# Optimization experiments

Measured on AMD Instinct MI355X. Metric: run time of the kernel, lower is better.

## Reference

```python
import jax, jax.numpy as jnp
import numpy as np
import math
from jax import lax

B, C, L = 8, 512, 1024
NCONV, K, H = 4, 7, 8
DH = C // H
EPS = 1e-5
NEG = -1e30


def layer_norm(x, g, b):
    mu = jnp.mean(x, axis=-1, keepdims=True)
    var = jnp.mean(jnp.square(x - mu), axis=-1, keepdims=True)
    return (x - mu) * lax.rsqrt(var + EPS) * g + b


def positional_encoding(d, n):
    pos = jnp.arange(n, dtype=jnp.float32)[:, None]                     # [n,1]
    div = jnp.exp(jnp.arange(0, d, 2, dtype=jnp.float32) * (-math.log(10000.0) / d))
    ang = pos * div                                                      # [n,d/2]
    pe = jnp.zeros((d, n), dtype=jnp.float32)
    pe = pe.at[0::2].set(jnp.sin(ang).T).at[1::2].set(jnp.cos(ang).T)
    return pe                                                            # [d,n]


def setup_inputs() -> dict:
    key = jax.random.key(0)
    ks = jax.random.split(key, 20)
    s = 0.02
    inp = {
        "x": jax.random.normal(ks[0], (B, C, L), jnp.float32),
        "mask": jnp.ones((B, L), jnp.float32),
        # conv stack params (stacked over NCONV layers)
        "dw_w": jax.random.normal(ks[1], (NCONV, C, 1, K), jnp.float32) * s,
        "dw_b": jnp.zeros((NCONV, C), jnp.float32),
        "pw_w": jax.random.normal(ks[2], (NCONV, C, C), jnp.float32) * s,
        "pw_b": jnp.zeros((NCONV, C), jnp.float32),
        "ln_conv_g": jnp.ones((NCONV, C), jnp.float32),
        "ln_conv_b": jnp.zeros((NCONV, C), jnp.float32),
        # attention params (torch Linear layout: [out,in])
        "Wq": jax.random.normal(ks[3], (C, C), jnp.float32) * s,
        "bq": jnp.zeros((C,), jnp.float32),
        "Wk": jax.random.normal(ks[4], (C, C), jnp.float32) * s,
        "bk": jnp.zeros((C,), jnp.float32),
        "Wv": jax.random.normal(ks[5], (C, C), jnp.float32) * s,
        "bv": jnp.zeros((C,), jnp.float32),
        "Wo": jax.random.normal(ks[6], (C, C), jnp.float32) * s,
        "bo": jnp.zeros((C,), jnp.float32),
        "ln_att_g": jnp.ones((C,), jnp.float32),
        "ln_att_b": jnp.zeros((C,), jnp.float32),
        # final fc + its layernorm
        "Wf": jax.random.normal(ks[7], (C, C), jnp.float32) * s,
        "bf": jnp.zeros((C,), jnp.float32),
        "ln_fc_g": jnp.ones((C,), jnp.float32),
        "ln_fc_b": jnp.zeros((C,), jnp.float32),
    }
    return inp


def reference(x, mask, dw_w, dw_b, pw_w, pw_b, ln_conv_g, ln_conv_b,
              Wq, bq, Wk, bk, Wv, bv, Wo, bo, ln_att_g, ln_att_b,
              Wf, bf, ln_fc_g, ln_fc_b):
    # positional encoding on channels-first input, then -> [B,L,C]
    out = x + positional_encoding(C, L)[None]          # [B,C,L]; dropout = eval mode (identity)
    out = out.transpose(0, 2, 1)                       # [B,L,C]
    res = out
    for i in range(NCONV):                             # fixed small layer loop
        h = layer_norm(out, ln_conv_g[i], ln_conv_b[i])
        h = h.transpose(0, 2, 1)                       # [B,C,L]
        h = lax.conv_general_dilated(h, dw_w[i], (1,), [(K // 2, K // 2)],
                                     dimension_numbers=("NCH", "OIH", "NCH"),
                                     feature_group_count=C) + dw_b[i][None, :, None]
        h = jnp.einsum("bcl,oc->bol", h, pw_w[i]) + pw_b[i][None, :, None]
        h = jax.nn.relu(h).transpose(0, 2, 1)          # [B,L,C]
        out = h + res
        res = out
    # masked multi-head self-attention
    a = layer_norm(out, ln_att_g, ln_att_b)
    q = (a @ Wq.T + bq).reshape(B, L, H, DH)
    k = (a @ Wk.T + bk).reshape(B, L, H, DH)
    v = (a @ Wv.T + bv).reshape(B, L, H, DH)
    scale = 1.0 / math.sqrt(DH)
    scores = jnp.einsum("blhd,bmhd->bhlm", q, k) * scale   # [B,H,L,L]
    m = mask[:, None, None, :]                              # mask over keys
    scores = scores * m + (1.0 - m) * NEG
    attn = jax.nn.softmax(scores, axis=-1)
    o = jnp.einsum("bhlm,bmhd->blhd", attn, v).reshape(B, L, C)
    o = o @ Wo.T + bo
    out = o + res
    res = out
    # feed-forward (single Linear + relu) with residual
    f = layer_norm(out, ln_fc_g, ln_fc_b)
    f = jax.nn.relu(f @ Wf.T + bf)
    out = f + res
    return out
```

## Files before the change

### kernel.cpp

```cpp
#include <hip/hip_runtime.h>
#include <hip/hip_bf16.h>

#define L_SEQ 1024
#define CCH   512
#define NB    8

typedef __bf16 bf16_t;
typedef __bf16 bf16x4 __attribute__((ext_vector_type(4)));
typedef __bf16 bf16x8 __attribute__((ext_vector_type(8)));
typedef float  f32x4  __attribute__((ext_vector_type(4)));

__device__ __forceinline__ void gload_lds16(const void* g, void* l) {
  __builtin_amdgcn_global_load_lds((const __attribute__((address_space(1))) void*)g,
                                   (__attribute__((address_space(3))) void*)l, 16, 0, 0);
}

__global__ __launch_bounds__(256) void cvtall_kernel(
    const float* __restrict__ pw_w, const float* __restrict__ Wq,
    const float* __restrict__ Wk, const float* __restrict__ Wv,
    const float* __restrict__ Wo, const float* __restrict__ Wf,
    const float* __restrict__ dw_w,
    bf16_t* __restrict__ WPW, bf16_t* __restrict__ WQKV,
    bf16_t* __restrict__ WOB, bf16_t* __restrict__ WFB,
    float* __restrict__ WT) {
  int idx = blockIdx.x * 256 + threadIdx.x;
  if (idx < 1048576) { WPW[idx] = (bf16_t)pw_w[idx]; return; }
  idx -= 1048576;
  if (idx < 262144) { WQKV[idx] = (bf16_t)Wq[idx]; return; }
  idx -= 262144;
  if (idx < 262144) { WQKV[262144 + idx] = (bf16_t)Wk[idx]; return; }
  idx -= 262144;
  if (idx < 262144) { WQKV[524288 + idx] = (bf16_t)Wv[idx]; return; }
  idx -= 262144;
  if (idx < 262144) { WOB[idx] = (bf16_t)Wo[idx]; return; }
  idx -= 262144;
  if (idx < 262144) { WFB[idx] = (bf16_t)Wf[idx]; return; }
  idx -= 262144;
  if (idx < 14336) {
    int i = idx / 3584, r = idx % 3584, t = r >> 9, c = r & 511;
    WT[idx] = dw_w[i * 3584 + c * 7 + t];
  }
}

__global__ __launch_bounds__(256) void pet_kernel(float* __restrict__ PET) {
  int idx = blockIdx.x * 256 + threadIdx.x;
  int l = idx >> 9, c = idx & 511;
  float div = expf(-(float)(2 * (c >> 1)) * (9.210340371976184f / 512.0f));
  float ang = (float)l * div;
  PET[idx] = (c & 1) ? cosf(ang) : sinf(ang);
}

__global__ __launch_bounds__(256) void pe_kernel(const float* __restrict__ x,
                                                 const float* __restrict__ PET,
                                                 float* __restrict__ out) {
  __shared__ float tile[32][33];
  int l0 = blockIdx.x * 32, c0 = blockIdx.y * 32, b = blockIdx.z;
  int tx = threadIdx.x, ty = threadIdx.y;
#pragma unroll
  for (int r = 0; r < 32; r += 8)
    tile[ty + r][tx] = x[(size_t)(b * CCH + c0 + ty + r) * L_SEQ + l0 + tx];
  __syncthreads();
#pragma unroll
  for (int r = 0; r < 32; r += 8) {
    int l = l0 + ty + r, c = c0 + tx;
    out[(size_t)(b * L_SEQ + l) * CCH + c] = tile[tx][ty + r] + PET[l * CCH + c];
  }
}

__global__ __launch_bounds__(256) void stats_kernel(const float* __restrict__ in,
                                                    float* __restrict__ Psum,
                                                    float* __restrict__ Psq) {
  int w = threadIdx.x >> 6, l = threadIdx.x & 63;
  int row = blockIdx.x * 4 + w;
  const float* p = in + (size_t)row * CCH + l * 8;
  float v[8];
  *(float4*)(&v[0]) = *(const float4*)p;
  *(float4*)(&v[4]) = *(const float4*)(p + 4);
  float s = 0.f, q = 0.f;
#pragma unroll
  for (int j = 0; j < 8; j++) { s += v[j]; q += v[j] * v[j]; }
  s += __shfl_xor(s, 1); q += __shfl_xor(q, 1);
  s += __shfl_xor(s, 2); q += __shfl_xor(q, 2);
  s += __shfl_xor(s, 4); q += __shfl_xor(q, 4);
  if ((l & 7) == 0) {
    Psum[row * 8 + (l >> 3)] = s;
    Psq[row * 8 + (l >> 3)] = q;
  }
}

__global__ __launch_bounds__(256) void ln_apply_kernel(const float* __restrict__ in,
                                                       const float* __restrict__ Psum,
                                                       const float* __restrict__ Psq,
                                                       const float* __restrict__ gam,
                                                       const float* __restrict__ bet,
                                                       bf16_t* __restrict__ out) {
  int w = threadIdx.x >> 6, l = threadIdx.x & 63;
  int row = blockIdx.x * 4 + w;
  float v0 = 0.f;
  if (l < 8) v0 = Psum[row * 8 + l];
  else if (l < 16) v0 = Psq[row * 8 + (l - 8)];
  v0 += __shfl_xor(v0, 1); v0 += __shfl_xor(v0, 2); v0 += __shfl_xor(v0, 4);
  float sum = __shfl(v0, 0), sq = __shfl(v0, 8);
  float mean = sum * (1.0f / 512.0f);
  float var = sq * (1.0f / 512.0f) - mean * mean;
  float inv = rsqrtf(var + 1e-5f);
  const float* p = in + (size_t)row * CCH + l * 8;
  float v[8], gv[8], bv[8];
  *(float4*)(&v[0]) = *(const float4*)p;
  *(float4*)(&v[4]) = *(const float4*)(p + 4);
  *(float4*)(&gv[0]) = *(const float4*)(gam + l * 8);
  *(float4*)(&gv[4]) = *(const float4*)(gam + l * 8 + 4);
  *(float4*)(&bv[0]) = *(const float4*)(bet + l * 8);
  *(float4*)(&bv[4]) = *(const float4*)(bet + l * 8 + 4);
  bf16x8 o;
#pragma unroll
  for (int j = 0; j < 8; j++) o[j] = (bf16_t)((v[j] - mean) * inv * gv[j] + bv[j]);
  *(bf16x8*)(out + (size_t)row * CCH + l * 8) = o;
}

__global__ __launch_bounds__(256) void dwln_kernel(const float* __restrict__ in,
                                                   const float* __restrict__ Psum,
                                                   const float* __restrict__ Psq,
                                                   const float* __restrict__ gam,
                                                   const float* __restrict__ bet,
                                                   const float* __restrict__ wtt,
                                                   const float* __restrict__ dbias,
                                                   bf16_t* __restrict__ out) {
  int idx = blockIdx.x * 256 + threadIdx.x;
  int lane = threadIdx.x & 63;
  int row = idx >> 6;
  int l = row & (L_SEQ - 1);
  float m_ = 0.f, i_ = 0.f;
  if (lane < 7) {
    int ll = l + lane - 3;
    if (ll >= 0 && ll < L_SEQ) {
      int rr = row + lane - 3;
      float s = 0.f, q = 0.f;
#pragma unroll
      for (int c = 0; c < 8; c++) { s += Psum[rr * 8 + c]; q += Psq[rr * 8 + c]; }
      float mm = s * (1.0f / 512.0f);
      m_ = mm;
      i_ = rsqrtf(q * (1.0f / 512.0f) - mm * mm + 1e-5f);
    }
  }
  float gv[8], bv[8], acc[8];
  *(float4*)&gv[0] = *(const float4*)(gam + lane * 8);
  *(float4*)&gv[4] = *(const float4*)(gam + lane * 8 + 4);
  *(float4*)&bv[0] = *(const float4*)(bet + lane * 8);
  *(float4*)&bv[4] = *(const float4*)(bet + lane * 8 + 4);
  *(float4*)&acc[0] = *(const float4*)(dbias + lane * 8);
  *(float4*)&acc[4] = *(const float4*)(dbias + lane * 8 + 4);
#pragma unroll
  for (int t = 0; t < 7; t++) {
    float mt = __shfl(m_, t), it = __shfl(i_, t);
    int ll = l + t - 3;
    if (ll >= 0 && ll < L_SEQ) {
      const float* p = in + (size_t)(row + t - 3) * CCH + lane * 8;
      float v[8], wv[8];
      *(float4*)&v[0] = *(const float4*)p;
      *(float4*)&v[4] = *(const float4*)(p + 4);
      *(float4*)&wv[0] = *(const float4*)(wtt + t * CCH + lane * 8);
      *(float4*)&wv[4] = *(const float4*)(wtt + t * CCH + lane * 8 + 4);
#pragma unroll
      for (int j = 0; j < 8; j++)
        acc[j] += ((v[j] - mt) * it * gv[j] + bv[j]) * wv[j];
    }
  }
  bf16x8 o;
#pragma unroll
  for (int j = 0; j < 8; j++) o[j] = (bf16_t)acc[j];
  *(bf16x8*)&out[(size_t)row * CCH + lane * 8] = o;
}

#define GEMM_STAGE(SRCA, SRCB, BI, K0)                                            \
  do {                                                                            \
    _Pragma("unroll") for (int cc = 0; cc < 2; cc++) {                            \
      int row_ = cc * 32 + w * 8 + srow;                                          \
      int off_ = (scb ^ ((row_ & 7) << 4)) >> 1;                                  \
      gload_lds16(SRCA + (size_t)(m0 + row_) * CCH + (K0) + off_,                 \
                  &As[BI][(cc * 32 + w * 8) * 64]);                               \
    }                                                                             \
    _Pragma("unroll") for (int cc = 0; cc < 4; cc++) {                            \
      int row_ = cc * 32 + w * 8 + srow;                                          \
      int off_ = (scb ^ ((row_ & 7) << 4)) >> 1;                                  \
      gload_lds16(SRCB + (size_t)(n0 + row_) * CCH + (K0) + off_,                 \
                  &Bs[BI][(cc * 32 + w * 8) * 64]);                               \
    }                                                                             \
  } while (0)

#define GEMM_COMPUTE(BI)                                                          \
  do {                                                                            \
    _Pragma("unroll") for (int ks = 0; ks < 2; ks++) {                            \
      bf16x8 fa[2], fb[4];                                                        \
      _Pragma("unroll") for (int i = 0; i < 2; i++) {                             \
        int ra = wr * 32 + i * 16 + lc;                                           \
        fa[i] = *(const bf16x8*)&As[BI][ra * 64 +                                 \
                 (((ks * 64 + lg * 16) ^ ((ra & 7) << 4)) >> 1)];                 \
      }                                                                           \
      _Pragma("unroll") for (int j = 0; j < 4; j++) {                             \
        int rb = wc * 64 + j * 16 + lc;                                           \
        fb[j] = *(const bf16x8*)&Bs[BI][rb * 64 +                                 \
                 (((ks * 64 + lg * 16) ^ ((rb & 7) << 4)) >> 1)];                 \
      }                                                                           \
      _Pragma("unroll") for (int i = 0; i < 2; i++)                               \
        _Pragma("unroll") for (int j = 0; j < 4; j++)                             \
          acc[i][j] = __builtin_amdgcn_mfma_f32_16x16x32_bf16(fa[i], fb[j],       \
                                                              acc[i][j], 0, 0, 0);\
    }                                                                             \
  } while (0)

template <int RELU, int RES, int BF16OUT, int STATS>
__global__ __launch_bounds__(256) void gemm_kernel(const bf16_t* __restrict__ A,
                                                   const bf16_t* __restrict__ W,
                                                   const float* __restrict__ bias,
                                                   const float* __restrict__ res,
                                                   float* __restrict__ outf,
                                                   bf16_t* __restrict__ outb,
                                                   float* __restrict__ Psum,
                                                   float* __restrict__ Psq) {
  __shared__ __align__(16) bf16_t As[2][64 * 64];
  __shared__ __align__(16) bf16_t Bs[2][128 * 64];
  int tid = threadIdx.x;
  int w = tid >> 6, l = tid & 63;
  int m0 = blockIdx.x * 64, n0 = blockIdx.y * 128;
  int wr = w >> 1, wc = w & 1;
  int lc = l & 15, lg = l >> 4;
  int srow = l >> 3, scb = (l & 7) * 16;
  f32x4 acc[2][4];
#pragma unroll
  for (int i = 0; i < 2; i++)
#pragma unroll
    for (int j = 0; j < 4; j++) acc[i][j] = f32x4{0.f, 0.f, 0.f, 0.f};

  GEMM_STAGE(A, W, 0, 0);
  __syncthreads();
  int cur = 0;
  for (int t = 0; t < 8; t++) {
    if (t < 7) GEMM_STAGE(A, W, cur ^ 1, (t + 1) * 64);
    GEMM_COMPUTE(cur);
    __syncthreads();
    cur ^= 1;
  }

  float ps[2][4], pq[2][4];
  if (STATS) {
#pragma unroll
    for (int i = 0; i < 2; i++)
#pragma unroll
      for (int r = 0; r < 4; r++) { ps[i][r] = 0.f; pq[i][r] = 0.f; }
  }
#pragma unroll
  for (int i = 0; i < 2; i++) {
    int mbase = m0 + wr * 32 + i * 16 + lg * 4;
#pragma unroll
    for (int j = 0; j < 4; j++) {
      int n = n0 + wc * 64 + j * 16 + lc;
      float bn = bias[n];
#pragma unroll
      for (int r = 0; r < 4; r++) {
        int m = mbase + r;
        float v2 = acc[i][j][r] + bn;
        if (RELU) v2 = fmaxf(v2, 0.f);
        if (RES) v2 += res[(size_t)m * CCH + n];
        if (BF16OUT) outb[(size_t)m * CCH + n] = (bf16_t)v2;
        else outf[(size_t)m * CCH + n] = v2;
        if (STATS) { ps[i][r] += v2; pq[i][r] += v2 * v2; }
      }
    }
  }
  if (STATS) {
    int chunk = blockIdx.y * 2 + wc;
#pragma unroll
    for (int i = 0; i < 2; i++)
#pragma unroll
      for (int r = 0; r < 4; r++) {
        float s = ps[i][r], q = pq[i][r];
        s += __shfl_xor(s, 1); q += __shfl_xor(q, 1);
        s += __shfl_xor(s, 2); q += __shfl_xor(q, 2);
        s += __shfl_xor(s, 4); q += __shfl_xor(q, 4);
        s += __shfl_xor(s, 8); q += __shfl_xor(q, 8);
        if (lc == 0) {
          int row = m0 + wr * 32 + i * 16 + lg * 4 + r;
          Psum[row * 8 + chunk] = s;
          Psq[row * 8 + chunk] = q;
        }
      }
  }
}

__global__ __launch_bounds__(256) void qkv_kernel(const bf16_t* __restrict__ A,
                                                  const bf16_t* __restrict__ Wqkv,
                                                  const float* __restrict__ bq,
                                                  const float* __restrict__ bk,
                                                  const float* __restrict__ bv,
                                                  bf16_t* __restrict__ QB,
                                                  bf16_t* __restrict__ KB,
                                                  bf16_t* __restrict__ VT) {
  __shared__ __align__(16) bf16_t As[2][64 * 64];
  __shared__ __align__(16) bf16_t Bs[2][128 * 64];
  int tid = threadIdx.x;
  int w = tid >> 6, l = tid & 63;
  int m0 = blockIdx.x * 64, n0 = blockIdx.y * 128;
  int sec = n0 >> 9;
  int wr = w >> 1, wc = w & 1;
  int lc = l & 15, lg = l >> 4;
  int srow = l >> 3, scb = (l & 7) * 16;
  f32x4 acc[2][4];
#pragma unroll
  for (int i = 0; i < 2; i++)
#pragma unroll
    for (int j = 0; j < 4; j++) acc[i][j] = f32x4{0.f, 0.f, 0.f, 0.f};

  GEMM_STAGE(A, Wqkv, 0, 0);
  __syncthreads();
  int cur = 0;
  for (int t = 0; t < 8; t++) {
    if (t < 7) GEMM_STAGE(A, Wqkv, cur ^ 1, (t + 1) * 64);
    GEMM_COMPUTE(cur);
    __syncthreads();
    cur ^= 1;
  }

  const float* bp = (sec == 0) ? bq : (sec == 1) ? bk : bv;
#pragma unroll
  for (int i = 0; i < 2; i++) {
    int mbase = m0 + wr * 32 + i * 16 + lg * 4;
#pragma unroll
    for (int j = 0; j < 4; j++) {
      int n = n0 + wc * 64 + j * 16 + lc;
      int nl = n & 511;
      float bn = bp[nl];
      if (sec < 2) {
        bf16_t* ob = (sec == 0) ? QB : KB;
#pragma unroll
        for (int r = 0; r < 4; r++)
          ob[(size_t)(mbase + r) * CCH + nl] = (bf16_t)(acc[i][j][r] + bn);
      } else {
        int h = nl >> 6, d = nl & 63;
        int b = mbase >> 10, lpos = mbase & 1023;
        bf16x4 t;
#pragma unroll
        for (int r = 0; r < 4; r++) t[r] = (bf16_t)(acc[i][j][r] + bn);
        *(bf16x4*)&VT[(((size_t)(b * 8 + h) * 64 + d) * L_SEQ) + lpos] = t;
      }
    }
  }
}

__global__ __launch_bounds__(256) void attn_kernel(const bf16_t* __restrict__ Q,
                                                   const bf16_t* __restrict__ K,
                                                   const bf16_t* __restrict__ VT,
                                                   const float* __restrict__ mask,
                                                   bf16_t* __restrict__ O) {
  __shared__ __align__(16) bf16_t Ks[64 * 64];
  __shared__ __align__(16) bf16_t Vs[64 * 64];
  __shared__ __align__(16) bf16_t Pl[4][16 * 64];
  int tid = threadIdx.x;
  int w = tid >> 6, l = tid & 63;
  int bid = blockIdx.x;
  int sw = (bid & 7) * 64 + (bid >> 3);
  int qb = sw & 7, h = (sw >> 3) & 7, b = sw >> 6;
  int lg = l >> 4, lc = l & 15;

  bf16x8 qf[2][2];
#pragma unroll
  for (int s = 0; s < 2; s++) {
    int qrow = qb * 128 + s * 64 + w * 16 + lc;
    const bf16_t* qptr = Q + ((size_t)(b * L_SEQ + qrow) * CCH + h * 64);
    qf[s][0] = *(const bf16x8*)(qptr + lg * 8);
    qf[s][1] = *(const bf16x8*)(qptr + 32 + lg * 8);
  }

  f32x4 oacc[2][4];
  float psl[2][4];
#pragma unroll
  for (int s = 0; s < 2; s++)
#pragma unroll
    for (int nf = 0; nf < 4; nf++) {
      oacc[s][nf] = f32x4{0.f, 0.f, 0.f, 0.f};
      psl[s][nf] = 0.f;
    }

  int srow = l >> 3;
  int scb = (l & 7) * 16;

  for (int kc = 0; kc < 16; kc++) {
#pragma unroll
    for (int r = 0; r < 2; r++) {
      int row = r * 32 + w * 8 + srow;
      int sc = (scb ^ ((row & 7) << 4)) >> 1;
      int key = kc * 64 + row;
      gload_lds16(K + ((size_t)(b * L_SEQ + key) * CCH + h * 64 + sc),
                  &Ks[(r * 32 + w * 8) * 64]);
      gload_lds16(VT + (((size_t)(b * 8 + h) * 64 + row) * L_SEQ + kc * 64 + sc),
                  &Vs[(r * 32 + w * 8) * 64]);
    }
    __syncthreads();

    float mv[4];
#pragma unroll
    for (int kf = 0; kf < 4; kf++) mv[kf] = mask[b * L_SEQ + kc * 64 + kf * 16 + lc];

#pragma unroll
    for (int s = 0; s < 2; s++) {
      f32x4 sacc[4];
#pragma unroll
      for (int kf = 0; kf < 4; kf++) sacc[kf] = f32x4{0.f, 0.f, 0.f, 0.f};
      __builtin_amdgcn_s_setprio(1);
#pragma unroll
      for (int kf = 0; kf < 4; kf++) {
        int row = kf * 16 + lc;
        int sx = (row & 7) << 4;
        const bf16_t* kr = &Ks[row * 64];
        bf16x8 b0 = *(const bf16x8*)(kr + (((lg * 16) ^ sx) >> 1));
        sacc[kf] = __builtin_amdgcn_mfma_f32_16x16x32_bf16(qf[s][0], b0, sacc[kf], 0, 0, 0);
        bf16x8 b1 = *(const bf16x8*)(kr + (((64 + lg * 16) ^ sx) >> 1));
        sacc[kf] = __builtin_amdgcn_mfma_f32_16x16x32_bf16(qf[s][1], b1, sacc[kf], 0, 0, 0);
      }
      __builtin_amdgcn_s_setprio(0);

#pragma unroll
      for (int kf = 0; kf < 4; kf++) {
        float mneg = (1.f - mv[kf]) * (-1e30f);
        float msc = 0.125f * mv[kf];
#pragma unroll
        for (int j = 0; j < 4; j++) {
          float p = __expf(sacc[kf][j] * msc + mneg);
          psl[s][j] += p;
          int q = lg * 4 + j;
          int cb = (kf * 32 + lc * 2) ^ ((q & 7) << 4);
          Pl[w][(q * 128 + cb) >> 1] = (bf16_t)p;
        }
      }

      int sp = (lc & 7) << 4;
      bf16x8 pa0 = *(const bf16x8*)&Pl[w][(lc * 128 + ((lg * 16) ^ sp)) >> 1];
      bf16x8 pa1 = *(const bf16x8*)&Pl[w][(lc * 128 + ((64 + lg * 16) ^ sp)) >> 1];
      __builtin_amdgcn_s_setprio(1);
#pragma unroll
      for (int nf = 0; nf < 4; nf++) {
        int d = nf * 16 + lc;
        int sx = (d & 7) << 4;
        const bf16_t* vr = &Vs[d * 64];
        bf16x8 vb0 = *(const bf16x8*)(vr + (((lg * 16) ^ sx) >> 1));
        oacc[s][nf] = __builtin_amdgcn_mfma_f32_16x16x32_bf16(pa0, vb0, oacc[s][nf], 0, 0, 0);
        bf16x8 vb1 = *(const bf16x8*)(vr + (((64 + lg * 16) ^ sx) >> 1));
        oacc[s][nf] = __builtin_amdgcn_mfma_f32_16x16x32_bf16(pa1, vb1, oacc[s][nf], 0, 0, 0);
      }
      __builtin_amdgcn_s_setprio(0);
    }
    __syncthreads();
  }

#pragma unroll
  for (int off = 1; off < 16; off <<= 1)
#pragma unroll
    for (int s = 0; s < 2; s++)
#pragma unroll
      for (int j = 0; j < 4; j++) psl[s][j] += __shfl_xor(psl[s][j], off);

#pragma unroll
  for (int s = 0; s < 2; s++)
#pragma unroll
    for (int j = 0; j < 4; j++) {
      float is = 1.0f / psl[s][j];
      int r = qb * 128 + s * 64 + w * 16 + lg * 4 + j;
      bf16_t* op = O + ((size_t)(b * L_SEQ + r) * CCH + h * 64);
#pragma unroll
      for (int nf = 0; nf < 4; nf++) op[nf * 16 + lc] = (bf16_t)(oacc[s][nf][j] * is);
    }
}

extern "C" void kernel_launch(void* const* d_in, const int* in_sizes, int n_in,
                              void* d_out, int out_size, void* d_ws, size_t ws_size,
                              hipStream_t stream) {
  const float* x = (const float*)d_in[0];
  const float* mask = (const float*)d_in[1];
  const float* dw_w = (const float*)d_in[2];
  const float* dw_b = (const float*)d_in[3];
  const float* pw_w = (const float*)d_in[4];
  const float* pw_b = (const float*)d_in[5];
  const float* ln_conv_g = (const float*)d_in[6];
  const float* ln_conv_b = (const float*)d_in[7];
  const float* Wq = (const float*)d_in[8];  const float* bq = (const float*)d_in[9];
  const float* Wk = (const float*)d_in[10]; const float* bk = (const float*)d_in[11];
  const float* Wv = (const float*)d_in[12]; const float* bv = (const float*)d_in[13];
  const float* Wo = (const float*)d_in[14]; const float* bo = (const float*)d_in[15];
  const float* ln_att_g = (const float*)d_in[16]; const float* ln_att_b = (const float*)d_in[17];
  const float* Wf = (const float*)d_in[18]; const float* bfc = (const float*)d_in[19];
  const float* ln_fc_g = (const float*)d_in[20]; const float* ln_fc_b = (const float*)d_in[21];

  float* OUT = (float*)d_out;

  char* ws = (char*)d_ws;
  bf16_t* ABF  = (bf16_t*)(ws);
  bf16_t* QB   = (bf16_t*)(ws + (8u << 20));
  bf16_t* KB   = (bf16_t*)(ws + (16u << 20));
  bf16_t* VT   = (bf16_t*)(ws + (24u << 20));
  char*   wb   = ws + (32u << 20);
  bf16_t* WPW  = (bf16_t*)(wb);
  bf16_t* WQKV = (bf16_t*)(wb + (2u << 20));
  bf16_t* WOB  = (bf16_t*)(wb + 3584u * 1024);
  bf16_t* WFB  = (bf16_t*)(wb + (4u << 20));
  float*  WT   = (float*)(wb + 4608u * 1024);
  float*  PET  = (float*)(ws + (37u << 20));
  float*  Psum = (float*)(ws + (39u << 20));
  float*  Psq  = (float*)(ws + (39u << 20) + 262144);

  cvtall_kernel<<<9272, 256, 0, stream>>>(pw_w, Wq, Wk, Wv, Wo, Wf, dw_w,
                                          WPW, WQKV, WOB, WFB, WT);
  pet_kernel<<<2048, 256, 0, stream>>>(PET);
  pe_kernel<<<dim3(32, 16, NB), dim3(32, 8), 0, stream>>>(x, PET, OUT);
  stats_kernel<<<2048, 256, 0, stream>>>(OUT, Psum, Psq);

  dim3 ggrid(128, 4);
  for (int i = 0; i < 4; i++) {
    dwln_kernel<<<2048, 256, 0, stream>>>(OUT, Psum, Psq, ln_conv_g + i * 512,
                                          ln_conv_b + i * 512, WT + i * 3584,
                                          dw_b + i * 512, ABF);
    gemm_kernel<1, 1, 0, 1><<<ggrid, 256, 0, stream>>>(ABF, WPW + i * 262144,
                                                       pw_b + i * 512, OUT, OUT,
                                                       nullptr, Psum, Psq);
  }
  ln_apply_kernel<<<2048, 256, 0, stream>>>(OUT, Psum, Psq, ln_att_g, ln_att_b, ABF);
  qkv_kernel<<<dim3(128, 12), 256, 0, stream>>>(ABF, WQKV, bq, bk, bv, QB, KB, VT);
  attn_kernel<<<512, 256, 0, stream>>>(QB, KB, VT, mask, ABF);
  gemm_kernel<0, 1, 0, 1><<<ggrid, 256, 0, stream>>>(ABF, WOB, bo, OUT, OUT,
                                                     nullptr, Psum, Psq);
  ln_apply_kernel<<<2048, 256, 0, stream>>>(OUT, Psum, Psq, ln_fc_g, ln_fc_b, ABF);
  gemm_kernel<1, 1, 0, 0><<<ggrid, 256, 0, stream>>>(ABF, WFB, bfc, OUT,
                                                     (float*)d_out, nullptr,
                                                     nullptr, nullptr);
}
```

Before: 356.4 us.

## Reshape GEMM tiles to 32x256, double-buffer attention K/V, fold PE table into conversion

The GEMM and QKV kernels move from a 64x128 tile with a 2x2 warp grid to a 32x256 tile where each of the four warps owns a 64-column strip, and the grids change to match. The attention kernel gains double-buffered K/V shared-memory tiles so the next key chunk loads while the current one is computed. The positional-encoding table is now built inside the weight-conversion kernel, which removes one launch. The new tile shape reuses each A row across more output columns but halves the row count, and the attention double buffer doubles its K/V shared memory, which may lower occupancy.

```diff
diff --git a/kernel.cpp b/kernel.cpp
--- a/kernel.cpp
+++ b/kernel.cpp
@@ -22,7 +22,7 @@
     const float* __restrict__ dw_w,
     bf16_t* __restrict__ WPW, bf16_t* __restrict__ WQKV,
     bf16_t* __restrict__ WOB, bf16_t* __restrict__ WFB,
-    float* __restrict__ WT) {
+    float* __restrict__ WT, float* __restrict__ PET) {
   int idx = blockIdx.x * 256 + threadIdx.x;
   if (idx < 1048576) { WPW[idx] = (bf16_t)pw_w[idx]; return; }
   idx -= 1048576;
@@ -39,15 +39,15 @@
   if (idx < 14336) {
     int i = idx / 3584, r = idx % 3584, t = r >> 9, c = r & 511;
     WT[idx] = dw_w[i * 3584 + c * 7 + t];
-  }
-}
-
-__global__ __launch_bounds__(256) void pet_kernel(float* __restrict__ PET) {
-  int idx = blockIdx.x * 256 + threadIdx.x;
-  int l = idx >> 9, c = idx & 511;
-  float div = expf(-(float)(2 * (c >> 1)) * (9.210340371976184f / 512.0f));
-  float ang = (float)l * div;
-  PET[idx] = (c & 1) ? cosf(ang) : sinf(ang);
+    return;
+  }
+  idx -= 14336;
+  if (idx < 524288) {
+    int l = idx >> 9, c = idx & 511;
+    float div = expf(-(float)(2 * (c >> 1)) * (9.210340371976184f / 512.0f));
+    float ang = (float)l * div;
+    PET[idx] = (c & 1) ? cosf(ang) : sinf(ang);
+  }
 }
 
 __global__ __launch_bounds__(256) void pe_kernel(const float* __restrict__ x,
@@ -174,13 +174,13 @@
 
 #define GEMM_STAGE(SRCA, SRCB, BI, K0)                                            \
   do {                                                                            \
-    _Pragma("unroll") for (int cc = 0; cc < 2; cc++) {                            \
-      int row_ = cc * 32 + w * 8 + srow;                                          \
+    {                                                                             \
+      int row_ = w * 8 + srow;                                                    \
       int off_ = (scb ^ ((row_ & 7) << 4)) >> 1;                                  \
       gload_lds16(SRCA + (size_t)(m0 + row_) * CCH + (K0) + off_,                 \
-                  &As[BI][(cc * 32 + w * 8) * 64]);                               \
+                  &As[BI][(w * 8) * 64]);                                         \
     }                                                                             \
-    _Pragma("unroll") for (int cc = 0; cc < 4; cc++) {                            \
+    _Pragma("unroll") for (int cc = 0; cc < 8; cc++) {                            \
       int row_ = cc * 32 + w * 8 + srow;                                          \
       int off_ = (scb ^ ((row_ & 7) << 4)) >> 1;                                  \
       gload_lds16(SRCB + (size_t)(n0 + row_) * CCH + (K0) + off_,                 \
@@ -193,12 +193,12 @@
     _Pragma("unroll") for (int ks = 0; ks < 2; ks++) {                            \
       bf16x8 fa[2], fb[4];                                                        \
       _Pragma("unroll") for (int i = 0; i < 2; i++) {                             \
-        int ra = wr * 32 + i * 16 + lc;                                           \
+        int ra = i * 16 + lc;                                                     \
         fa[i] = *(const bf16x8*)&As[BI][ra * 64 +                                 \
                  (((ks * 64 + lg * 16) ^ ((ra & 7) << 4)) >> 1)];                 \
       }                                                                           \
       _Pragma("unroll") for (int j = 0; j < 4; j++) {                             \
-        int rb = wc * 64 + j * 16 + lc;                                           \
+        int rb = w * 64 + j * 16 + lc;                                            \
         fb[j] = *(const bf16x8*)&Bs[BI][rb * 64 +                                 \
                  (((ks * 64 + lg * 16) ^ ((rb & 7) << 4)) >> 1)];                 \
       }                                                                           \
@@ -218,12 +218,11 @@
                                                    bf16_t* __restrict__ outb,
                                                    float* __restrict__ Psum,
                                                    float* __restrict__ Psq) {
-  __shared__ __align__(16) bf16_t As[2][64 * 64];
-  __shared__ __align__(16) bf16_t Bs[2][128 * 64];
+  __shared__ __align__(16) bf16_t As[2][32 * 64];
+  __shared__ __align__(16) bf16_t Bs[2][256 * 64];
   int tid = threadIdx.x;
   int w = tid >> 6, l = tid & 63;
-  int m0 = blockIdx.x * 64, n0 = blockIdx.y * 128;
-  int wr = w >> 1, wc = w & 1;
+  int m0 = blockIdx.x * 32, n0 = blockIdx.y * 256;
   int lc = l & 15, lg = l >> 4;
   int srow = l >> 3, scb = (l & 7) * 16;
   f32x4 acc[2][4];
@@ -251,10 +250,10 @@
   }
 #pragma unroll
   for (int i = 0; i < 2; i++) {
-    int mbase = m0 + wr * 32 + i * 16 + lg * 4;
+    int mbase = m0 + i * 16 + lg * 4;
 #pragma unroll
     for (int j = 0; j < 4; j++) {
-      int n = n0 + wc * 64 + j * 16 + lc;
+      int n = n0 + w * 64 + j * 16 + lc;
       float bn = bias[n];
 #pragma unroll
       for (int r = 0; r < 4; r++) {
@@ -269,7 +268,7 @@
     }
   }
   if (STATS) {
-    int chunk = blockIdx.y * 2 + wc;
+    int chunk = blockIdx.y * 4 + w;
 #pragma unroll
     for (int i = 0; i < 2; i++)
 #pragma unroll
@@ -280,7 +279,7 @@
         s += __shfl_xor(s, 4); q += __shfl_xor(q, 4);
         s += __shfl_xor(s, 8); q += __shfl_xor(q, 8);
         if (lc == 0) {
-          int row = m0 + wr * 32 + i * 16 + lg * 4 + r;
+          int row = m0 + i * 16 + lg * 4 + r;
           Psum[row * 8 + chunk] = s;
           Psq[row * 8 + chunk] = q;
         }
@@ -296,13 +295,12 @@
                                                   bf16_t* __restrict__ QB,
                                                   bf16_t* __restrict__ KB,
                                                   bf16_t* __restrict__ VT) {
-  __shared__ __align__(16) bf16_t As[2][64 * 64];
-  __shared__ __align__(16) bf16_t Bs[2][128 * 64];
+  __shared__ __align__(16) bf16_t As[2][32 * 64];
+  __shared__ __align__(16) bf16_t Bs[2][256 * 64];
   int tid = threadIdx.x;
   int w = tid >> 6, l = tid & 63;
-  int m0 = blockIdx.x * 64, n0 = blockIdx.y * 128;
+  int m0 = blockIdx.x * 32, n0 = blockIdx.y * 256;
   int sec = n0 >> 9;
-  int wr = w >> 1, wc = w & 1;
   int lc = l & 15, lg = l >> 4;
   int srow = l >> 3, scb = (l & 7) * 16;
   f32x4 acc[2][4];
@@ -324,10 +322,10 @@
   const float* bp = (sec == 0) ? bq : (sec == 1) ? bk : bv;
 #pragma unroll
   for (int i = 0; i < 2; i++) {
-    int mbase = m0 + wr * 32 + i * 16 + lg * 4;
+    int mbase = m0 + i * 16 + lg * 4;
 #pragma unroll
     for (int j = 0; j < 4; j++) {
-      int n = n0 + wc * 64 + j * 16 + lc;
+      int n = n0 + w * 64 + j * 16 + lc;
       int nl = n & 511;
       float bn = bp[nl];
       if (sec < 2) {
@@ -347,13 +345,26 @@
   }
 }
 
+#define ATT_STAGE(BI, KC)                                                         \
+  do {                                                                            \
+    _Pragma("unroll") for (int r = 0; r < 2; r++) {                               \
+      int row = r * 32 + w * 8 + srow;                                            \
+      int sc = (scb ^ ((row & 7) << 4)) >> 1;                                     \
+      int key = (KC) * 64 + row;                                                  \
+      gload_lds16(K + ((size_t)(b * L_SEQ + key) * CCH + h * 64 + sc),            \
+                  &Ks[BI][(r * 32 + w * 8) * 64]);                                \
+      gload_lds16(VT + (((size_t)(b * 8 + h) * 64 + row) * L_SEQ + (KC) * 64 + sc),\
+                  &Vs[BI][(r * 32 + w * 8) * 64]);                                \
+    }                                                                             \
+  } while (0)
+
 __global__ __launch_bounds__(256) void attn_kernel(const bf16_t* __restrict__ Q,
                                                    const bf16_t* __restrict__ K,
                                                    const bf16_t* __restrict__ VT,
                                                    const float* __restrict__ mask,
                                                    bf16_t* __restrict__ O) {
-  __shared__ __align__(16) bf16_t Ks[64 * 64];
-  __shared__ __align__(16) bf16_t Vs[64 * 64];
+  __shared__ __align__(16) bf16_t Ks[2][64 * 64];
+  __shared__ __align__(16) bf16_t Vs[2][64 * 64];
   __shared__ __align__(16) bf16_t Pl[4][16 * 64];
   int tid = threadIdx.x;
   int w = tid >> 6, l = tid & 63;
@@ -384,18 +395,11 @@
   int srow = l >> 3;
   int scb = (l & 7) * 16;
 
+  ATT_STAGE(0, 0);
+  __syncthreads();
+  int cur = 0;
   for (int kc = 0; kc < 16; kc++) {
-#pragma unroll
-    for (int r = 0; r < 2; r++) {
-      int row = r * 32 + w * 8 + srow;
-      int sc = (scb ^ ((row & 7) << 4)) >> 1;
-      int key = kc * 64 + row;
-      gload_lds16(K + ((size_t)(b * L_SEQ + key) * CCH + h * 64 + sc),
-                  &Ks[(r * 32 + w * 8) * 64]);
-      gload_lds16(VT + (((size_t)(b * 8 + h) * 64 + row) * L_SEQ + kc * 64 + sc),
-                  &Vs[(r * 32 + w * 8) * 64]);
-    }
-    __syncthreads();
+    if (kc < 15) ATT_STAGE(cur ^ 1, kc + 1);
 
     float mv[4];
 #pragma unroll
@@ -411,7 +415,7 @@
       for (int kf = 0; kf < 4; kf++) {
         int row = kf * 16 + lc;
         int sx = (row & 7) << 4;
-        const bf16_t* kr = &Ks[row * 64];
+        const bf16_t* kr = &Ks[cur][row * 64];
         bf16x8 b0 = *(const bf16x8*)(kr + (((lg * 16) ^ sx) >> 1));
         sacc[kf] = __builtin_amdgcn_mfma_f32_16x16x32_bf16(qf[s][0], b0, sacc[kf], 0, 0, 0);
         bf16x8 b1 = *(const bf16x8*)(kr + (((64 + lg * 16) ^ sx) >> 1));
@@ -441,7 +445,7 @@
       for (int nf = 0; nf < 4; nf++) {
         int d = nf * 16 + lc;
         int sx = (d & 7) << 4;
-        const bf16_t* vr = &Vs[d * 64];
+        const bf16_t* vr = &Vs[cur][d * 64];
         bf16x8 vb0 = *(const bf16x8*)(vr + (((lg * 16) ^ sx) >> 1));
         oacc[s][nf] = __builtin_amdgcn_mfma_f32_16x16x32_bf16(pa0, vb0, oacc[s][nf], 0, 0, 0);
         bf16x8 vb1 = *(const bf16x8*)(vr + (((64 + lg * 16) ^ sx) >> 1));
@@ -450,6 +454,7 @@
       __builtin_amdgcn_s_setprio(0);
     }
     __syncthreads();
+    cur ^= 1;
   }
 
 #pragma unroll
@@ -507,13 +512,12 @@
   float*  Psum = (float*)(ws + (39u << 20));
   float*  Psq  = (float*)(ws + (39u << 20) + 262144);
 
-  cvtall_kernel<<<9272, 256, 0, stream>>>(pw_w, Wq, Wk, Wv, Wo, Wf, dw_w,
-                                          WPW, WQKV, WOB, WFB, WT);
-  pet_kernel<<<2048, 256, 0, stream>>>(PET);
+  cvtall_kernel<<<11320, 256, 0, stream>>>(pw_w, Wq, Wk, Wv, Wo, Wf, dw_w,
+                                           WPW, WQKV, WOB, WFB, WT, PET);
   pe_kernel<<<dim3(32, 16, NB), dim3(32, 8), 0, stream>>>(x, PET, OUT);
   stats_kernel<<<2048, 256, 0, stream>>>(OUT, Psum, Psq);
 
-  dim3 ggrid(128, 4);
+  dim3 ggrid(256, 2);
   for (int i = 0; i < 4; i++) {
     dwln_kernel<<<2048, 256, 0, stream>>>(OUT, Psum, Psq, ln_conv_g + i * 512,
                                           ln_conv_b + i * 512, WT + i * 3584,
@@ -523,7 +527,7 @@
                                                        nullptr, Psum, Psq);
   }
   ln_apply_kernel<<<2048, 256, 0, stream>>>(OUT, Psum, Psq, ln_att_g, ln_att_b, ABF);
-  qkv_kernel<<<dim3(128, 12), 256, 0, stream>>>(ABF, WQKV, bq, bk, bv, QB, KB, VT);
+  qkv_kernel<<<dim3(256, 6), 256, 0, stream>>>(ABF, WQKV, bq, bk, bv, QB, KB, VT);
   attn_kernel<<<512, 256, 0, stream>>>(QB, KB, VT, mask, ABF);
   gemm_kernel<0, 1, 0, 1><<<ggrid, 256, 0, stream>>>(ABF, WOB, bo, OUT, OUT,
                                                      nullptr, Psum, Psq);
```

New measurement: 359.2 us. About the same (+0.8%).
